# Kernel tuning notes

Measured on AMD Instinct MI355X. Metric: run time of the kernel, lower is better.

Reference implementation:

```python
import jax, jax.numpy as jnp
import numpy as np

HEADS = 4
DIM_HEAD = 32
DIM = 256
EPS = 1e-12


def setup_inputs() -> dict:
    key = jax.random.key(0)
    ks = jax.random.split(key, 4)
    b, c, n = 8, DIM, 16384
    hidden = HEADS * DIM_HEAD  # 128
    x = jax.random.normal(ks[0], (b, c, n), dtype=jnp.float32)
    w_qkv = jax.random.normal(ks[1], (hidden * 3, c), dtype=jnp.float32) * (1.0 / np.sqrt(c))
    w_out = jax.random.normal(ks[2], (c, hidden), dtype=jnp.float32) * (1.0 / np.sqrt(hidden))
    b_out = jax.random.normal(ks[3], (c,), dtype=jnp.float32) * 0.01
    g = jnp.ones((1, c, 1), dtype=jnp.float32)
    return {"x": x, "w_qkv": w_qkv, "w_out": w_out, "b_out": b_out, "g": g}


def reference(x, w_qkv, w_out, b_out, g):
    b, c, n = x.shape
    scale = DIM_HEAD ** -0.5
    # to_qkv: Conv1d kernel-size 1, no bias == channel matmul
    qkv = jnp.einsum('oc,bcn->bon', w_qkv, x)  # [b, 3*h*d, n]
    q, k, v = jnp.split(qkv, 3, axis=1)
    def to_heads(t):
        return t.reshape(b, HEADS, DIM_HEAD, n)  # b (h d) n -> b h d n
    q, k, v = to_heads(q), to_heads(k), to_heads(v)
    q = jax.nn.softmax(q, axis=-2) * scale      # softmax over d
    k = jax.nn.softmax(k, axis=-1)              # softmax over n
    context = jnp.einsum('bhdn,bhen->bhde', k, v)  # [b,h,d,e]
    out = jnp.einsum('bhde,bhdn->bhen', context, q)  # [b,h,e,n]
    out = out.reshape(b, HEADS * DIM_HEAD, n)   # b h d n -> b (h d) n
    # to_out Conv1d (kernel 1) with bias
    out = jnp.einsum('oc,bcn->bon', w_out, out) + b_out[None, :, None]
    # RMSNorm: F.normalize over channel dim * g * sqrt(c)
    norm = jnp.sqrt(jnp.sum(out * out, axis=1, keepdims=True))
    out = out / jnp.maximum(norm, EPS) * g * jnp.sqrt(jnp.asarray(c, out.dtype))
    return out
```

## Files before the change

kernel.cpp:

```cpp
#include <hip/hip_runtime.h>
#include <hip/hip_bf16.h>
#include <math.h>

#define B_    8
#define C_    256
#define N_    16384
#define H_    4
#define D_    32
#define HID_  128
#define ROWS_ 384
#define SCALE 0.17677669529663687f

typedef __attribute__((ext_vector_type(8))) short bf16x8;
typedef __attribute__((ext_vector_type(16))) float f32x16;

__device__ __forceinline__ short f2bf(float f) {
    union { __hip_bfloat16 h; short s; } u;
    u.h = __float2bfloat16(f);
    return u.s;
}
__device__ __forceinline__ float bf2f(short s) {
    union { unsigned u; float f; } x;
    x.u = ((unsigned)(unsigned short)s) << 16;
    return x.f;
}

__global__ __launch_bounds__(256) void k_conv(
    const float* __restrict__ wqkv, const float* __restrict__ wout,
    short* __restrict__ wrearr, short* __restrict__ woutb)
{
    int i = blockIdx.x * 256 + threadIdx.x;
    if (i < 12288) {
        int tile = i >> 10;
        int ks   = (i >> 6) & 15;
        int l    = i & 63;
        int row  = tile * 32 + (l & 31);
        int k0   = ks * 16 + (l >> 5) * 8;
        const float* src = wqkv + row * 256 + k0;
        float4 f0 = *(const float4*)(src);
        float4 f1 = *(const float4*)(src + 4);
        short o[8] = {f2bf(f0.x), f2bf(f0.y), f2bf(f0.z), f2bf(f0.w),
                      f2bf(f1.x), f2bf(f1.y), f2bf(f1.z), f2bf(f1.w)};
        *(uint4*)(wrearr + (size_t)i * 8) = *(uint4*)o;
    } else {
        int j = (i - 12288) * 4;
        float4 f = *(const float4*)(wout + j);
        short4 s; s.x = f2bf(f.x); s.y = f2bf(f.y); s.z = f2bf(f.z); s.w = f2bf(f.w);
        *(short4*)(woutb + j) = s;
    }
}

__global__ __launch_bounds__(256, 4) void k_qkv(
    const float* __restrict__ x, const short* __restrict__ wrearr,
    short* __restrict__ qtb, short* __restrict__ part16,
    float* __restrict__ partden)
{
    __shared__ __align__(16) char smA[32768];

    const int blk = blockIdx.x;
    const int b   = blk >> 8;
    const int n0  = (blk & 255) << 6;
    const int t   = threadIdx.x;
    const int l   = t & 63;
    const int wv  = t >> 6;
    const int c31 = l & 31;
    const int hf  = l >> 5;

    {
        const int kg = t >> 4;
        const int n4 = (t & 15) * 4;
        const float* xb = x + (size_t)b * C_ * N_ + n0 + n4;
#pragma unroll
        for (int it = 0; it < 4; it++) {
            const int k = it * 64 + kg * 4;
            const float* xp = xb + (size_t)k * N_;
            float4 r0 = *(const float4*)(xp);
            float4 r1 = *(const float4*)(xp + N_);
            float4 r2 = *(const float4*)(xp + 2 * (size_t)N_);
            float4 r3 = *(const float4*)(xp + 3 * (size_t)N_);
#define WRT(J, FLD) { short4 sv; sv.x = f2bf(r0.FLD); sv.y = f2bf(r1.FLD); \
    sv.z = f2bf(r2.FLD); sv.w = f2bf(r3.FLD); \
    int n_ = n4 + J; int ad_ = n_ * 512 + ((2 * k) ^ ((n_ & 31) << 4)); \
    *(short4*)(smA + ad_) = sv; }
            WRT(0, x) WRT(1, y) WRT(2, z) WRT(3, w)
#undef WRT
        }
    }
    __syncthreads();

    f32x16 acc[3][2];
#pragma unroll
    for (int ti = 0; ti < 3; ti++)
#pragma unroll
        for (int ct = 0; ct < 2; ct++)
#pragma unroll
            for (int r = 0; r < 16; r++) acc[ti][ct][r] = 0.f;

    const bf16x8* wp = (const bf16x8*)wrearr + (size_t)wv * 1024 + l;
    bf16x8 afN0 = wp[0], afN1 = wp[4096], afN2 = wp[8192];
#pragma unroll
    for (int ks = 0; ks < 16; ks++) {
        bf16x8 af0 = afN0, af1 = afN1, af2 = afN2;
        if (ks < 15) {
            afN0 = wp[(ks + 1) * 64];
            afN1 = wp[4096 + (ks + 1) * 64];
            afN2 = wp[8192 + (ks + 1) * 64];
        }
        const int slot = 2 * ks + hf;
        bf16x8 bfr0 = *(const bf16x8*)(smA + (c31)      * 512 + 16 * (slot ^ c31));
        bf16x8 bfr1 = *(const bf16x8*)(smA + (c31 + 32) * 512 + 16 * (slot ^ c31));
        acc[0][0] = __builtin_amdgcn_mfma_f32_32x32x16_bf16(af0, bfr0, acc[0][0], 0, 0, 0);
        acc[0][1] = __builtin_amdgcn_mfma_f32_32x32x16_bf16(af0, bfr1, acc[0][1], 0, 0, 0);
        acc[1][0] = __builtin_amdgcn_mfma_f32_32x32x16_bf16(af1, bfr0, acc[1][0], 0, 0, 0);
        acc[1][1] = __builtin_amdgcn_mfma_f32_32x32x16_bf16(af1, bfr1, acc[1][1], 0, 0, 0);
        acc[2][0] = __builtin_amdgcn_mfma_f32_32x32x16_bf16(af2, bfr0, acc[2][0], 0, 0, 0);
        acc[2][1] = __builtin_amdgcn_mfma_f32_32x32x16_bf16(af2, bfr1, acc[2][1], 0, 0, 0);
    }


#pragma unroll
    for (int ct = 0; ct < 2; ct++) {
        float mx = -1e30f;
#pragma unroll
        for (int r = 0; r < 16; r++) mx = fmaxf(mx, acc[0][ct][r]);
        mx = fmaxf(mx, __shfl_xor(mx, 32));
        float e[16]; float s = 0.f;
#pragma unroll
        for (int r = 0; r < 16; r++) { e[r] = __expf(acc[0][ct][r] - mx); s += e[r]; }
        s += __shfl_xor(s, 32);
        float inv = SCALE / s;
        short* qp = qtb + ((size_t)b * HID_ + wv * 32) * N_ + n0 + ct * 32 + c31;
#pragma unroll
        for (int r = 0; r < 16; r++) {
            int rm = (r & 3) + 8 * (r >> 2) + 4 * hf;
            qp[(size_t)rm * N_] = f2bf(e[r] * inv);
        }
    }
    __syncthreads();

    char* ekb = smA + wv * 8192;
    char* vvb = ekb + 4096;
#pragma unroll
    for (int ct = 0; ct < 2; ct++)
#pragma unroll
        for (int r = 0; r < 16; r++) {
            int rm = (r & 3) + 8 * (r >> 2) + 4 * hf;
            int n  = ct * 32 + c31;
            int ad = rm * 128 + ((2 * n) ^ ((rm & 7) << 4));
            *(short*)(ekb + ad) = f2bf(__expf(acc[1][ct][r]));
            *(short*)(vvb + ad) = f2bf(acc[2][ct][r]);
        }
    __syncthreads();

    f32x16 cD, dD;
#pragma unroll
    for (int r = 0; r < 16; r++) { cD[r] = 0.f; dD[r] = 0.f; }
    bf16x8 ones;
#pragma unroll
    for (int i = 0; i < 8; i++) ones[i] = (short)0x3F80;
#pragma unroll
    for (int ks = 0; ks < 4; ks++) {
        int slot = 2 * ks + hf;
        bf16x8 ea = *(const bf16x8*)(ekb + c31 * 128 + 16 * (slot ^ (c31 & 7)));
        bf16x8 vb = *(const bf16x8*)(vvb + c31 * 128 + 16 * (slot ^ (c31 & 7)));
        cD = __builtin_amdgcn_mfma_f32_32x32x16_bf16(ea, vb,   cD, 0, 0, 0);
        dD = __builtin_amdgcn_mfma_f32_32x32x16_bf16(ea, ones, dD, 0, 0, 0);
    }

    short* pb = part16 + ((size_t)blk * 4 + wv) * 1024;
#pragma unroll
    for (int r = 0; r < 16; r++) {
        int rm = (r & 3) + 8 * (r >> 2) + 4 * hf;
        pb[rm * 32 + c31] = f2bf(cD[r]);
    }
    if (c31 == 0) {
        float* pd = partden + ((size_t)blk * 4 + wv) * 32;
#pragma unroll
        for (int r = 0; r < 16; r++) {
            int rm = (r & 3) + 8 * (r >> 2) + 4 * hf;
            pd[rm] = dD[r];
        }
    }
}

__global__ __launch_bounds__(256) void k_red(
    const short* __restrict__ part16, const float* __restrict__ partden,
    short* __restrict__ ctxbf)
{
    __shared__ float den_s[32];
    const int bh = blockIdx.x;
    const int b  = bh >> 2, h = bh & 3;
    const int t  = threadIdx.x;
    const int d  = t >> 3;
    const int e4 = (t & 7) * 4;

    const short* p0 = part16 + ((size_t)(b * 256) * 4 + h) * 1024 + d * 32 + e4;
    float s0 = 0.f, s1 = 0.f, s2 = 0.f, s3 = 0.f;
    for (int q = 0; q < 256; q++) {
        short4 v = *(const short4*)(p0 + (size_t)q * 4096);
        s0 += bf2f(v.x); s1 += bf2f(v.y); s2 += bf2f(v.z); s3 += bf2f(v.w);
    }
    if ((t & 7) == 0) {
        const float* pd = partden + ((size_t)(b * 256) * 4 + h) * 32 + d;
        float ds = 0.f;
        for (int q = 0; q < 256; q++) ds += pd[(size_t)q * 128];
        den_s[d] = ds;
    }
    __syncthreads();
    float inv = 1.0f / den_s[d];
    short* cb = ctxbf + (size_t)bh * 1024 + d;
    cb[(e4 + 0) * 32] = f2bf(s0 * inv);
    cb[(e4 + 1) * 32] = f2bf(s1 * inv);
    cb[(e4 + 2) * 32] = f2bf(s2 * inv);
    cb[(e4 + 3) * 32] = f2bf(s3 * inv);
}

__global__ __launch_bounds__(256, 3) void k_out(
    const short* __restrict__ qtb, const short* __restrict__ ctxbf,
    const short* __restrict__ woutb, const float* __restrict__ bout,
    const float* __restrict__ g, float* __restrict__ out)
{
    __shared__ __align__(16) char  hidS[16384];
    __shared__ float gl[C_], bl[C_];
    __shared__ float red[4][64];
    __shared__ float nrm[64];

    const int blk = blockIdx.x;
    const int b   = blk >> 8;
    const int n0  = (blk & 255) << 6;
    const int t   = threadIdx.x;
    const int l   = t & 63;
    const int wv  = t >> 6;
    const int c31 = l & 31;
    const int hf  = l >> 5;

    gl[t] = g[t];
    bl[t] = bout[t];
    __syncthreads();

    f32x16 hD[2];
#pragma unroll
    for (int ct = 0; ct < 2; ct++)
#pragma unroll
        for (int r = 0; r < 16; r++) hD[ct][r] = 0.f;
    const short* qb = qtb + (size_t)b * HID_ * N_ + n0;
    const short* cb = ctxbf + ((size_t)(b * H_ + wv) * 32 + c31) * 32;
#pragma unroll
    for (int ks = 0; ks < 2; ks++) {
        int k0 = ks * 16 + hf * 8;
        bf16x8 af = *(const bf16x8*)(cb + k0);
#pragma unroll
        for (int ct = 0; ct < 2; ct++) {
            bf16x8 bq;
#pragma unroll
            for (int i = 0; i < 8; i++)
                bq[i] = qb[(size_t)(wv * 32 + k0 + i) * N_ + ct * 32 + c31];
            hD[ct] = __builtin_amdgcn_mfma_f32_32x32x16_bf16(af, bq, hD[ct], 0, 0, 0);
        }
    }
#pragma unroll
    for (int ct = 0; ct < 2; ct++)
#pragma unroll
        for (int r = 0; r < 16; r++) {
            int rm = (r & 3) + 8 * (r >> 2) + 4 * hf;
            int hfull = wv * 32 + rm;
            int n = ct * 32 + c31;
            int ad = n * 256 + ((2 * hfull) ^ ((n & 15) << 4));
            *(short*)(hidS + ad) = f2bf(hD[ct][r]);
        }
    __syncthreads();

    f32x16 yacc[2][2];
#pragma unroll
    for (int rt = 0; rt < 2; rt++)
#pragma unroll
        for (int ct = 0; ct < 2; ct++)
#pragma unroll
            for (int r = 0; r < 16; r++) yacc[rt][ct][r] = 0.f;

#pragma unroll
    for (int ks = 0; ks < 8; ks++) {
        int k0 = ks * 16 + hf * 8;
        int sx = 2 * ks + hf;
        bf16x8 bq0 = *(const bf16x8*)(hidS + (c31)      * 256 + 16 * (sx ^ (c31 & 15)));
        bf16x8 bq1 = *(const bf16x8*)(hidS + (c31 + 32) * 256 + 16 * (sx ^ (c31 & 15)));
#pragma unroll
        for (int rt = 0; rt < 2; rt++) {
            bf16x8 af = *(const bf16x8*)(woutb + (wv * 64 + rt * 32 + c31) * HID_ + k0);
            yacc[rt][0] = __builtin_amdgcn_mfma_f32_32x32x16_bf16(af, bq0, yacc[rt][0], 0, 0, 0);
            yacc[rt][1] = __builtin_amdgcn_mfma_f32_32x32x16_bf16(af, bq1, yacc[rt][1], 0, 0, 0);
        }
    }

#pragma unroll
    for (int rt = 0; rt < 2; rt++)
#pragma unroll
        for (int r = 0; r < 16; r++) {
            int rm = (r & 3) + 8 * (r >> 2) + 4 * hf;
            float bo = bl[wv * 64 + rt * 32 + rm];
            yacc[rt][0][r] += bo;
            yacc[rt][1][r] += bo;
        }
#pragma unroll
    for (int ct = 0; ct < 2; ct++) {
        float s = 0.f;
#pragma unroll
        for (int rt = 0; rt < 2; rt++)
#pragma unroll
            for (int r = 0; r < 16; r++) s = fmaf(yacc[rt][ct][r], yacc[rt][ct][r], s);
        s += __shfl_xor(s, 32);
        if (hf == 0) red[wv][ct * 32 + c31] = s;
    }
    __syncthreads();
    if (t < 64) {
        float S = red[0][t] + red[1][t] + red[2][t] + red[3][t];
        nrm[t] = 16.0f / fmaxf(sqrtf(S), 1e-12f);
    }
    __syncthreads();

    float* ob = out + (size_t)b * C_ * N_ + n0;
#pragma unroll
    for (int rt = 0; rt < 2; rt++)
#pragma unroll
        for (int r = 0; r < 16; r++) {
            int rm = (r & 3) + 8 * (r >> 2) + 4 * hf;
            int c  = wv * 64 + rt * 32 + rm;
            float gc = gl[c];
#pragma unroll
            for (int ct = 0; ct < 2; ct++) {
                int n = ct * 32 + c31;
                ob[(size_t)c * N_ + n] = yacc[rt][ct][r] * gc * nrm[n];
            }
        }
}

extern "C" void kernel_launch(void* const* d_in, const int* in_sizes, int n_in,
                              void* d_out, int out_size, void* d_ws, size_t ws_size,
                              hipStream_t stream)
{
    const float* x    = (const float*)d_in[0];
    const float* wqkv = (const float*)d_in[1];
    const float* wout = (const float*)d_in[2];
    const float* bout = (const float*)d_in[3];
    const float* g    = (const float*)d_in[4];
    float* out = (float*)d_out;

    short* qtb     = (short*)d_ws;
    short* part16  = qtb + (size_t)B_ * N_ * HID_;
    float* partden = (float*)(part16 + (size_t)2048 * 4 * 1024);
    short* ctxbf   = (short*)(partden + (size_t)2048 * 4 * 32);
    short* wrearr  = ctxbf + (size_t)B_ * H_ * 32 * 32;
    short* woutb   = wrearr + (size_t)12288 * 8;

    k_conv<<<80, 256, 0, stream>>>(wqkv, wout, wrearr, woutb);
    k_qkv<<<B_ * (N_ / 64), 256, 0, stream>>>(x, wrearr, qtb, part16, partden);
    k_red<<<B_ * H_, 256, 0, stream>>>(part16, partden, ctxbf);
    k_out<<<B_ * (N_ / 64), 256, 0, stream>>>(qtb, ctxbf, woutb, bout, g, out);
}
```

Baseline: 140.7 us.

## Widen QKV projection blocks to 128 columns with XCD-aware block swizzle

k_qkv now runs 512-thread blocks over 128 sequence columns with a 64KB LDS tile instead of 256 threads over 64 columns. Each pair of waves shares one head's weight fragments across two column halves. The block index is remapped so consecutive blocks land on different batches, which is meant to keep each XCD's L2 traffic to one batch. One barrier before the per-wave context MFMA is removed, since each wave only reads its own LDS region. The larger LDS footprint per block may lower how many blocks fit on a CU.

```diff
diff --git a/kernel.cpp b/kernel.cpp
--- a/kernel.cpp
+++ b/kernel.cpp
@@ -50,26 +50,30 @@
     }
 }
 
-__global__ __launch_bounds__(256, 4) void k_qkv(
+__global__ __launch_bounds__(512, 4) void k_qkv(
     const float* __restrict__ x, const short* __restrict__ wrearr,
     short* __restrict__ qtb, short* __restrict__ part16,
     float* __restrict__ partden)
 {
-    __shared__ __align__(16) char smA[32768];
-
-    const int blk = blockIdx.x;
-    const int b   = blk >> 8;
-    const int n0  = (blk & 255) << 6;
-    const int t   = threadIdx.x;
-    const int l   = t & 63;
-    const int wv  = t >> 6;
-    const int c31 = l & 31;
-    const int hf  = l >> 5;
+    __shared__ __align__(16) char smA[65536];
+
+    const int orig = blockIdx.x;
+    const int swz  = (orig & 7) * 128 + (orig >> 3);
+    const int b    = swz >> 7;
+    const int nwin = swz & 127;
+    const int nb   = nwin << 7;
+    const int t    = threadIdx.x;
+    const int l    = t & 63;
+    const int wv   = t >> 6;
+    const int h    = wv & 3;
+    const int ch   = wv >> 2;
+    const int c31  = l & 31;
+    const int hf   = l >> 5;
 
     {
-        const int kg = t >> 4;
-        const int n4 = (t & 15) * 4;
-        const float* xb = x + (size_t)b * C_ * N_ + n0 + n4;
+        const int kg = t >> 5;
+        const int n4 = (t & 31) * 4;
+        const float* xb = x + (size_t)b * C_ * N_ + nb + n4;
 #pragma unroll
         for (int it = 0; it < 4; it++) {
             const int k = it * 64 + kg * 4;
@@ -96,8 +100,10 @@
 #pragma unroll
             for (int r = 0; r < 16; r++) acc[ti][ct][r] = 0.f;
 
-    const bf16x8* wp = (const bf16x8*)wrearr + (size_t)wv * 1024 + l;
+    const bf16x8* wp = (const bf16x8*)wrearr + (size_t)h * 1024 + l;
     bf16x8 afN0 = wp[0], afN1 = wp[4096], afN2 = wp[8192];
+    const char* smB0 = smA + (ch * 64 + c31) * 512;
+    const char* smB1 = smA + (ch * 64 + 32 + c31) * 512;
 #pragma unroll
     for (int ks = 0; ks < 16; ks++) {
         bf16x8 af0 = afN0, af1 = afN1, af2 = afN2;
@@ -107,8 +113,8 @@
             afN2 = wp[8192 + (ks + 1) * 64];
         }
         const int slot = 2 * ks + hf;
-        bf16x8 bfr0 = *(const bf16x8*)(smA + (c31)      * 512 + 16 * (slot ^ c31));
-        bf16x8 bfr1 = *(const bf16x8*)(smA + (c31 + 32) * 512 + 16 * (slot ^ c31));
+        bf16x8 bfr0 = *(const bf16x8*)(smB0 + 16 * (slot ^ c31));
+        bf16x8 bfr1 = *(const bf16x8*)(smB1 + 16 * (slot ^ c31));
         acc[0][0] = __builtin_amdgcn_mfma_f32_32x32x16_bf16(af0, bfr0, acc[0][0], 0, 0, 0);
         acc[0][1] = __builtin_amdgcn_mfma_f32_32x32x16_bf16(af0, bfr1, acc[0][1], 0, 0, 0);
         acc[1][0] = __builtin_amdgcn_mfma_f32_32x32x16_bf16(af1, bfr0, acc[1][0], 0, 0, 0);
@@ -129,7 +135,7 @@
         for (int r = 0; r < 16; r++) { e[r] = __expf(acc[0][ct][r] - mx); s += e[r]; }
         s += __shfl_xor(s, 32);
         float inv = SCALE / s;
-        short* qp = qtb + ((size_t)b * HID_ + wv * 32) * N_ + n0 + ct * 32 + c31;
+        short* qp = qtb + ((size_t)b * HID_ + h * 32) * N_ + nb + ch * 64 + ct * 32 + c31;
 #pragma unroll
         for (int r = 0; r < 16; r++) {
             int rm = (r & 3) + 8 * (r >> 2) + 4 * hf;
@@ -150,7 +156,6 @@
             *(short*)(ekb + ad) = f2bf(__expf(acc[1][ct][r]));
             *(short*)(vvb + ad) = f2bf(acc[2][ct][r]);
         }
-    __syncthreads();
 
     f32x16 cD, dD;
 #pragma unroll
@@ -167,14 +172,15 @@
         dD = __builtin_amdgcn_mfma_f32_32x32x16_bf16(ea, ones, dD, 0, 0, 0);
     }
 
-    short* pb = part16 + ((size_t)blk * 4 + wv) * 1024;
+    const int q64 = nwin * 2 + ch;
+    short* pb = part16 + ((size_t)(b * 256 + q64) * 4 + h) * 1024;
 #pragma unroll
     for (int r = 0; r < 16; r++) {
         int rm = (r & 3) + 8 * (r >> 2) + 4 * hf;
         pb[rm * 32 + c31] = f2bf(cD[r]);
     }
     if (c31 == 0) {
-        float* pd = partden + ((size_t)blk * 4 + wv) * 32;
+        float* pd = partden + ((size_t)(b * 256 + q64) * 4 + h) * 32;
 #pragma unroll
         for (int r = 0; r < 16; r++) {
             int rm = (r & 3) + 8 * (r >> 2) + 4 * hf;
@@ -353,7 +359,7 @@
     short* woutb   = wrearr + (size_t)12288 * 8;
 
     k_conv<<<80, 256, 0, stream>>>(wqkv, wout, wrearr, woutb);
-    k_qkv<<<B_ * (N_ / 64), 256, 0, stream>>>(x, wrearr, qtb, part16, partden);
+    k_qkv<<<1024, 512, 0, stream>>>(x, wrearr, qtb, part16, partden);
     k_red<<<B_ * H_, 256, 0, stream>>>(part16, partden, ctxbf);
     k_out<<<B_ * (N_ / 64), 256, 0, stream>>>(qtb, ctxbf, woutb, bout, g, out);
 }
```

Result: faster. 137.4 us (-2.3%).
